# Performance work log

Hardware: AMD Instinct MI355X
Metric: run time of the kernel (lower is better)

The kernel has to match this reference:

```python
import jax, jax.numpy as jnp
import numpy as np

B, T, D_IN, D_SAE, K = 256, 8, 768, 8192, 32


def setup_inputs() -> dict:
    key = jax.random.key(0)
    k1, k2, k3 = jax.random.split(key, 3)
    x = jax.random.normal(k1, (B, T, D_IN), dtype=jnp.float32)
    # kaiming_uniform: bound = sqrt(6 / fan_in), fan_in = prod of trailing dims
    bound_e = float(np.sqrt(6.0 / (D_SAE * D_IN)))
    W_enc = jax.random.uniform(k2, (T, D_SAE, D_IN), jnp.float32, -bound_e, bound_e)
    bound_d = float(np.sqrt(6.0 / (D_IN * D_SAE)))
    W_dec = jax.random.uniform(k3, (T, D_IN, D_SAE), jnp.float32, -bound_d, bound_d)
    # decoder column normalization (norm over d_in axis), as in _normalize_decoder
    norms = jnp.clip(jnp.linalg.norm(W_dec, axis=1, keepdims=True), 1e-8)
    W_dec = W_dec / norms
    b_enc = jnp.zeros((T, D_SAE), jnp.float32)
    b_dec = jnp.zeros((T, D_IN), jnp.float32)
    return {"x": x, "W_enc": W_enc, "b_enc": b_enc, "W_dec": W_dec,
            "b_dec": b_dec, "k": K}


def reference(x, W_enc, b_enc, W_dec, b_dec, k):
    # x: (B, T, d_in)
    x_c = x - b_dec[None]                                   # (B, T, d)
    pre = jnp.einsum('btd,thd->bth', x_c, W_enc) + b_enc[None]  # (B, T, h)
    bt = pre.shape[0] * pre.shape[1]
    pre_flat = pre.reshape(bt, -1)
    topk_vals, topk_idx = jax.lax.top_k(pre_flat, k)        # (BT, k)
    rows = jnp.arange(bt)[:, None]
    u_flat = jnp.zeros_like(pre_flat).at[rows, topk_idx].set(jax.nn.relu(topk_vals))
    u = u_flat.reshape(pre.shape)                            # (B, T, h)
    x_hat = jnp.einsum('bth,tdh->btd', u, W_dec) + b_dec[None]
    recon_loss = jnp.mean(jnp.sum((x_hat - x) ** 2, axis=-1))
    return recon_loss, x_hat, u
```

## Files before the change

kernel.cpp:

```cpp
#include <hip/hip_runtime.h>
#include <cstdint>
#include <cstddef>

constexpr int B_SZ  = 256;
constexpr int T_SZ  = 8;
constexpr int DIN   = 768;
constexpr int DSAE  = 8192;
constexpr int KSEL  = 32;
constexpr int NROWS = B_SZ * T_SZ;
constexpr int CAND_CAP = 64;
constexpr int RCAP  = 32;
constexpr float EPS_W = 3.2e-4f;
constexpr int NSK   = DIN / 32;

constexpr size_t XC_SZ    = (size_t)NROWS * DIN;
constexpr size_t OFF_XC   = 0;
constexpr size_t OFF_XCP  = OFF_XC + XC_SZ;
constexpr size_t XCP_W    = XC_SZ / 2;
constexpr size_t OFF_SIDX = OFF_XCP + XCP_W;
constexpr size_t OFF_SVAL = OFF_SIDX + (size_t)NROWS * KSEL;
constexpr size_t OFF_BIG  = OFF_SVAL + (size_t)NROWS * KSEL;
constexpr size_t BIG_W    = (size_t)T_SZ * DSAE * DIN / 2;
constexpr size_t WS_FAST_WORDS = OFF_BIG + BIG_W;

typedef short bf16x8 __attribute__((ext_vector_type(8)));
typedef float f32x4  __attribute__((ext_vector_type(4)));

__device__ inline unsigned rne1(float x) {
  unsigned u = __float_as_uint(x);
  return (u + 0x7FFFu + ((u >> 16) & 1u)) >> 16;
}
__device__ inline float bf16tof(unsigned short v) {
  return __uint_as_float((unsigned)v << 16);
}
__device__ inline unsigned packtr(float a, float b) {
  return (__float_as_uint(a) >> 16) | (__float_as_uint(b) & 0xFFFF0000u);
}
__device__ inline void gload_lds16(const void* g, void* l) {
  __builtin_amdgcn_global_load_lds(
      (const __attribute__((address_space(1))) void*)g,
      (__attribute__((address_space(3))) void*)l, 16, 0, 0);
}

__global__ void k_zero(float* p) { *p = 0.f; }

__global__ __launch_bounds__(256) void k_xc(const float* __restrict__ x,
                                            const float* __restrict__ bdec,
                                            float* __restrict__ xc,
                                            unsigned short* __restrict__ xcp) {
  const int c = blockIdx.x * 256 + threadIdx.x;
  const int lane = c & 63;
  const int u = c >> 6;
  const int s  = u % NSK;
  const int tt = (u / NSK) & (T_SZ - 1);
  const int gm = u / (NSK * T_SZ);
  const int b  = gm * 16 + (lane & 15);
  const int k0 = s * 32 + (lane >> 4) * 8;
  const size_t rowOff = ((size_t)(b * T_SZ + tt)) * DIN + k0;
  float4 v0 = *(const float4*)(x + rowOff);
  float4 v1 = *(const float4*)(x + rowOff + 4);
  float4 d0 = *(const float4*)(bdec + tt * DIN + k0);
  float4 d1 = *(const float4*)(bdec + tt * DIN + k0 + 4);
  v0.x -= d0.x; v0.y -= d0.y; v0.z -= d0.z; v0.w -= d0.w;
  v1.x -= d1.x; v1.y -= d1.y; v1.z -= d1.z; v1.w -= d1.w;
  *(float4*)(xc + rowOff) = v0;
  *(float4*)(xc + rowOff + 4) = v1;
  uint4 p;
  p.x = rne1(v0.x) | (rne1(v0.y) << 16);
  p.y = rne1(v0.z) | (rne1(v0.w) << 16);
  p.z = rne1(v1.x) | (rne1(v1.y) << 16);
  p.w = rne1(v1.z) | (rne1(v1.w) << 16);
  *(uint4*)(xcp + (size_t)c * 8) = p;
}

__global__ __launch_bounds__(256, 2) void k_encoder(const unsigned short* __restrict__ xcp,
                                                    const float* __restrict__ Wenc,
                                                    const float* __restrict__ benc,
                                                    float* __restrict__ pre) {
  __shared__ __align__(16) float Bs[4][64 * 32];
  const int tid = threadIdx.x;
  const int wm = tid >> 6, lane = tid & 63;
  const int l15 = lane & 15, kc = lane >> 4;

  int gRow[2], gCol[2], ldsL[2];
#pragma unroll
  for (int i = 0; i < 2; ++i) {
    int L = i * 4096 + tid * 16;
    int G = L ^ (((L >> 7) & 7) << 4);
    gRow[i] = G >> 7;
    gCol[i] = (G & 127) >> 2;
    ldsL[i] = L;
  }
  int bOff0[4], bOff1[4];
#pragma unroll
  for (int ni = 0; ni < 4; ++ni) {
    int row = ni * 16 + l15;
    int P = row * 128 + kc * 32;
    int sw = (row & 7) << 4;
    bOff0[ni] = P ^ sw;
    bOff1[ni] = (P + 16) ^ sw;
  }
  constexpr size_t A_MI = (size_t)T_SZ * NSK * 512;

  for (int tile = 0; tile < 2; ++tile) {
    const int tileId = blockIdx.x + tile * 512;
    const int t  = tileId >> 7;
    const int n0 = (tileId & 127) * 64;

    const float* bG = Wenc + ((size_t)t * DSAE + n0) * DIN;
    const unsigned short* aP =
        xcp + ((size_t)(wm * 4 * T_SZ + t) * NSK) * 512 + lane * 8;

    auto STAGE = [&](int buf, int s) {
#pragma unroll
      for (int i = 0; i < 2; ++i)
        gload_lds16(bG + (size_t)gRow[i] * DIN + s * 32 + gCol[i],
                    (char*)&Bs[0][0] + buf * 8192 + ldsL[i]);
    };

    f32x4 acc[4][4] = {};
    bf16x8 aA[4], aB[4];
    STAGE(0, 0);
#pragma unroll
    for (int mi = 0; mi < 4; ++mi)
      aA[mi] = *(const bf16x8*)(aP + mi * A_MI);
    STAGE(1, 1);

#define ENC_W6 asm volatile("s_waitcnt vmcnt(6)" ::: "memory")
#define ENC_W4 asm volatile("s_waitcnt vmcnt(4)" ::: "memory")
#define ENC_W0 asm volatile("s_waitcnt vmcnt(0)" ::: "memory")
#define ENC_STEP(u, PFB, PFA, WAITOP) do {                                   \
    if (PFB) STAGE(((u) + 2) & 3, s0 + (u) + 2);                             \
    if (PFA) {                                                               \
      const unsigned short* ap = aP + (size_t)(s0 + (u) + 1) * 512;          \
      _Pragma("unroll")                                                      \
      for (int mi = 0; mi < 4; ++mi) {                                       \
        bf16x8 v = *(const bf16x8*)(ap + mi * A_MI);                         \
        if ((u) % 2 == 0) aB[mi] = v; else aA[mi] = v;                       \
      }                                                                      \
    }                                                                        \
    __builtin_amdgcn_sched_barrier(0);                                       \
    WAITOP;                                                                  \
    __builtin_amdgcn_s_barrier();                                            \
    __builtin_amdgcn_sched_barrier(0);                                       \
    {                                                                        \
      const char* bb = (const char*)&Bs[0][0] + ((u) & 3) * 8192;            \
      _Pragma("unroll")                                                      \
      for (int ni = 0; ni < 4; ++ni) {                                       \
        f32x4 f0 = *(const f32x4*)(bb + bOff0[ni]);                          \
        f32x4 f1 = *(const f32x4*)(bb + bOff1[ni]);                          \
        union { uint32_t w[4]; bf16x8 h; } cvu;                              \
        cvu.w[0] = packtr(f0.x, f0.y); cvu.w[1] = packtr(f0.z, f0.w);        \
        cvu.w[2] = packtr(f1.x, f1.y); cvu.w[3] = packtr(f1.z, f1.w);        \
        _Pragma("unroll")                                                    \
        for (int mi = 0; mi < 4; ++mi)                                       \
          acc[mi][ni] = __builtin_amdgcn_mfma_f32_16x16x32_bf16(             \
              ((u) % 2 == 0) ? aA[mi] : aB[mi], cvu.h, acc[mi][ni], 0, 0, 0);\
      }                                                                      \
    }                                                                        \
  } while (0)

    int s0 = 0;
    for (int g = 0; g < 5; ++g, s0 += 4) {
      ENC_STEP(0, true, true, ENC_W6); ENC_STEP(1, true, true, ENC_W6);
      ENC_STEP(2, true, true, ENC_W6); ENC_STEP(3, true, true, ENC_W6);
    }
    ENC_STEP(0, true, true, ENC_W6);  ENC_STEP(1, true, true, ENC_W6);
    ENC_STEP(2, false, true, ENC_W4); ENC_STEP(3, false, false, ENC_W0);
#undef ENC_STEP
#undef ENC_W6
#undef ENC_W4
#undef ENC_W0

#pragma unroll
    for (int ni = 0; ni < 4; ++ni) {
      const int col = n0 + ni * 16 + l15;
      const float bias = benc[(size_t)t * DSAE + col];
#pragma unroll
      for (int mi = 0; mi < 4; ++mi) {
        const int rbase = wm * 64 + mi * 16 + kc * 4;
#pragma unroll
        for (int j = 0; j < 4; ++j)
          pre[((size_t)(rbase + j) * T_SZ + t) * DSAE + col] = acc[mi][ni][j] + bias;
      }
    }
    if (tile == 0) __syncthreads();
  }
}

__global__ __launch_bounds__(256) void k_select(const float* __restrict__ xc,
                                                const float* __restrict__ Wenc,
                                                const float* __restrict__ benc,
                                                float* u,
                                                int* __restrict__ sel_idx,
                                                float* __restrict__ sel_val) {
  const int r = blockIdx.x, t = r & (T_SZ - 1);
  __shared__ float sp[DSAE];
  __shared__ float redf[4], redf2[4];
  __shared__ int   redi[4];
  __shared__ float cv[CAND_CAP]; __shared__ int ci[CAND_CAP];
  __shared__ float sv[CAND_CAP]; __shared__ int si[CAND_CAP];
  __shared__ float rv[RCAP];     __shared__ int ri[RCAP];
  __shared__ double rd[RCAP];
  __shared__ double xd[DIN];
  __shared__ int   s_n, s_nR, s_A, s_nW;
  const int tid = threadIdx.x, lane = tid & 63, w = tid >> 6;
  float* urow = u + (size_t)r * DSAE;

  float s1 = 0.f, s2 = 0.f;
  for (int sgm = 0; sgm < DSAE / 256; ++sgm) {
    float v = urow[tid + sgm * 256];
    sp[tid + sgm * 256] = v;
    s1 += v; s2 = fmaf(v, v, s2);
  }
  for (int off = 32; off; off >>= 1) {
    s1 += __shfl_down(s1, off); s2 += __shfl_down(s2, off);
  }
  if (lane == 0) { redf[w] = s1; redf2[w] = s2; }
  __syncthreads();
  const float mean = (redf[0] + redf[1] + redf[2] + redf[3]) * (1.f / DSAE);
  const float var  = (redf2[0] + redf2[1] + redf2[2] + redf2[3]) * (1.f / DSAE) - mean * mean;
  const float sd   = sqrtf(fmaxf(var, 1e-20f));

  auto countGE = [&](float th) -> int {
    int c = 0;
#pragma unroll
    for (int sgm = 0; sgm < DSAE / 256; ++sgm)
      c += (sp[tid + sgm * 256] >= th) ? 1 : 0;
    for (int off = 32; off; off >>= 1) c += __shfl_down(c, off);
    __syncthreads();
    if (lane == 0) redi[w] = c;
    __syncthreads();
    return redi[0] + redi[1] + redi[2] + redi[3];
  };

  float tlo = mean + 2.0f * sd, thi = mean + 3.5f * sd;
  for (int it = 0; it < 8 && countGE(tlo) < KSEL; ++it) tlo -= sd;
  float th = mean + 2.52f * sd;
  int c = countGE(th);
  for (int it = 0; it < 24 && (c < KSEL || c > CAND_CAP); ++it) {
    if (c > CAND_CAP) tlo = th; else thi = th;
    th = 0.5f * (tlo + thi);
    c = countGE(th);
  }
  if (c < KSEL) { th = tlo; c = countGE(th); }

  if (tid == 0) s_n = 0;
  __syncthreads();
  for (int sgm = 0; sgm < DSAE / 256; ++sgm) {
    int i = tid + sgm * 256;
    float v = sp[i];
    if (v >= th) {
      int p = atomicAdd(&s_n, 1);
      if (p < CAND_CAP) { cv[p] = v; ci[p] = i; }
    }
  }
  __syncthreads();
  const int n = s_n < CAND_CAP ? s_n : CAND_CAP;

  if (tid < n) {
    float v = cv[tid]; int id = ci[tid];
    int rk = 0;
    for (int j = 0; j < n; ++j) {
      float vj = cv[j];
      rk += (vj > v || (vj == v && ci[j] < id)) ? 1 : 0;
    }
    sv[rk] = v; si[rk] = id;
  }
  __syncthreads();

  const float v32 = sv[KSEL - 1];
  const float wlo = v32 - EPS_W, whi = v32 + EPS_W;
  if (tid == 0) {
    int A = 0;
    while (A < KSEL - 1 && sv[A] > whi) ++A;
    s_A = A;
    int e = A;
    while (e < n && sv[e] >= wlo) ++e;
    s_nW = e - A;
  }
  __syncthreads();
  const int A  = s_A;
  const int nW = s_nW < RCAP ? s_nW : RCAP;
  if (tid < nW) { rv[tid] = sv[A + tid]; ri[tid] = si[A + tid]; }
  if (tid == 0) s_nR = nW;
  __syncthreads();
  if (th > wlo) {
    for (int sgm = 0; sgm < DSAE / 256; ++sgm) {
      int i = tid + sgm * 256;
      float v = sp[i];
      if (v >= wlo && v < th) {
        int p = atomicAdd(&s_nR, 1);
        if (p < RCAP) { rv[p] = v; ri[p] = i; }
      }
    }
  }
  __syncthreads();
  const int nR = s_nR < RCAP ? s_nR : RCAP;

  if (nR >= 2) {
    for (int i = tid; i < DIN; i += 256) xd[i] = (double)xc[(size_t)r * DIN + i];
    __syncthreads();
    for (int j = w; j < nR; j += 4) {
      const int h = ri[j];
      const float* wrow = Wenc + ((size_t)t * DSAE + h) * DIN;
      double s = 0.0;
#pragma unroll
      for (int ss = 0; ss < DIN / 64; ++ss)
        s += xd[lane + 64 * ss] * (double)wrow[lane + 64 * ss];
      for (int off = 32; off; off >>= 1) s += __shfl_down(s, off);
      if (lane == 0) rd[j] = s + (double)benc[(size_t)t * DSAE + h];
    }
  } else if (nR == 1) {
    if (tid == 0) rd[0] = (double)rv[0];
  }
  __syncthreads();

  for (int sgm = 0; sgm < DSAE / 256; ++sgm) urow[tid + sgm * 256] = 0.f;
  __syncthreads();

  if (tid < A) {
    float val = fmaxf(sv[tid], 0.f);
    urow[si[tid]] = val;
    sel_idx[(size_t)r * KSEL + tid] = si[tid];
    sel_val[(size_t)r * KSEL + tid] = val;
  }
  const int need = KSEL - A;
  if (tid < nR) {
    double v = rd[tid]; int id = ri[tid];
    int rk = 0;
    for (int j = 0; j < nR; ++j) {
      double vj = rd[j];
      rk += (vj > v || (vj == v && ri[j] < id)) ? 1 : 0;
    }
    if (rk < need) {
      float val = fmaxf((float)v, 0.f);
      urow[id] = val;
      sel_idx[(size_t)r * KSEL + A + rk] = id;
      sel_val[(size_t)r * KSEL + A + rk] = val;
    }
  }
}

__global__ __launch_bounds__(256) void k_transpose(const float* __restrict__ W,
                                                   unsigned short* __restrict__ Wt) {
  __shared__ unsigned short tile[128 * 137];
  const int h0 = blockIdx.x * 128;
  const int d0 = blockIdx.y * 128;
  const int t  = blockIdx.z;
  const int tid = threadIdx.x;
  const float* src = W + ((size_t)t * DIN + d0) * DSAE + h0;

#pragma unroll
  for (int i = 0; i < 16; ++i) {
    const int F = (i * 256 + tid) * 4;
    const int r = F >> 7, c = F & 127;
    float4 v = *(const float4*)(src + (size_t)r * DSAE + c);
    unsigned short* p = &tile[r * 137 + c];
    p[0] = (unsigned short)rne1(v.x); p[1] = (unsigned short)rne1(v.y);
    p[2] = (unsigned short)rne1(v.z); p[3] = (unsigned short)rne1(v.w);
  }
  __syncthreads();

#pragma unroll
  for (int j = 0; j < 16; ++j) {
    const int E  = j * 256 + tid;
    const int hr = E >> 5;
    const int dc = (E & 31) * 4;
    unsigned a = (unsigned)tile[(dc + 0) * 137 + hr] |
                 ((unsigned)tile[(dc + 1) * 137 + hr] << 16);
    unsigned b = (unsigned)tile[(dc + 2) * 137 + hr] |
                 ((unsigned)tile[(dc + 3) * 137 + hr] << 16);
    uint2 o; o.x = a; o.y = b;
    *(uint2*)(Wt + ((size_t)(t * DSAE + h0 + hr)) * DIN + d0 + dc) = o;
  }
}

template <bool TRANSPOSED>
__global__ __launch_bounds__(256) void k_decoder(const void* __restrict__ Wd_,
                                                 const float* __restrict__ x,
                                                 const float* __restrict__ bdec,
                                                 const int* __restrict__ sel_idx,
                                                 const float* __restrict__ sel_val,
                                                 float* __restrict__ xhat,
                                                 float* __restrict__ loss) {
  const int r = blockIdx.x, t = r & (T_SZ - 1);
  __shared__ int   si[KSEL];
  __shared__ float sv[KSEL];
  __shared__ float rbuf[4];
  const int tid = threadIdx.x;
  if (tid < KSEL) {
    si[tid] = sel_idx[(size_t)r * KSEL + tid] & (DSAE - 1);
    sv[tid] = sel_val[(size_t)r * KSEL + tid];
  }
  __syncthreads();

  float acc[3];
#pragma unroll
  for (int i = 0; i < 3; ++i) acc[i] = bdec[(size_t)t * DIN + tid + 256 * i];
#pragma unroll 4
  for (int j = 0; j < KSEL; ++j) {
    const int h = si[j];
    const float v = sv[j];
    if (TRANSPOSED) {
      const unsigned short* wrow =
          (const unsigned short*)Wd_ + ((size_t)t * DSAE + h) * DIN;
#pragma unroll
      for (int i = 0; i < 3; ++i)
        acc[i] = fmaf(v, bf16tof(wrow[tid + 256 * i]), acc[i]);
    } else {
      const float* Wd = (const float*)Wd_;
#pragma unroll
      for (int i = 0; i < 3; ++i)
        acc[i] = fmaf(v, Wd[((size_t)t * DIN + tid + 256 * i) * DSAE + h], acc[i]);
    }
  }
  float sq = 0.f;
#pragma unroll
  for (int i = 0; i < 3; ++i) {
    const int d = tid + 256 * i;
    const float xv = x[(size_t)r * DIN + d];
    xhat[(size_t)r * DIN + d] = acc[i];
    const float e = acc[i] - xv;
    sq = fmaf(e, e, sq);
  }
  for (int off = 32; off; off >>= 1) sq += __shfl_down(sq, off);
  if ((tid & 63) == 0) rbuf[tid >> 6] = sq;
  __syncthreads();
  if (tid == 0)
    atomicAdd(loss, (rbuf[0] + rbuf[1] + rbuf[2] + rbuf[3]) * (1.0f / NROWS));
}

extern "C" void kernel_launch(void* const* d_in, const int* in_sizes, int n_in,
                              void* d_out, int out_size, void* d_ws, size_t ws_size,
                              hipStream_t stream) {
  const float* x    = (const float*)d_in[0];
  const float* Wenc = (const float*)d_in[1];
  const float* benc = (const float*)d_in[2];
  const float* Wdec = (const float*)d_in[3];
  const float* bdec = (const float*)d_in[4];

  float* out  = (float*)d_out;
  float* loss = out;
  float* xhat = out + 1;
  float* u    = out + 1 + (size_t)NROWS * DIN;

  float*          wsf  = (float*)d_ws;
  float*          xc   = wsf + OFF_XC;
  unsigned short* xcp  = (unsigned short*)(wsf + OFF_XCP);
  int*            sidx = (int*)(wsf + OFF_SIDX);
  float*          sval = wsf + OFF_SVAL;
  unsigned short* big  = (unsigned short*)(wsf + OFF_BIG);
  const bool fast = ws_size >= WS_FAST_WORDS * sizeof(float);

  k_zero<<<1, 1, 0, stream>>>(loss);
  k_xc<<<NROWS * DIN / (256 * 8), 256, 0, stream>>>(x, bdec, xc, xcp);
  k_encoder<<<512, 256, 0, stream>>>(xcp, Wenc, benc, u);
  k_select<<<NROWS, 256, 0, stream>>>(xc, Wenc, benc, u, sidx, sval);
  if (fast) {
    k_transpose<<<dim3(DSAE / 128, DIN / 128, T_SZ), 256, 0, stream>>>(Wdec, big);
    k_decoder<true><<<NROWS, 256, 0, stream>>>(big, x, bdec, sidx, sval, xhat, loss);
  } else {
    k_decoder<false><<<NROWS, 256, 0, stream>>>(Wdec, x, bdec, sidx, sval, xhat, loss);
  }
}
```

Baseline: 239.4 us.

## Store encoder pre-activations as bf16 scratch and zero u in separate kernel

The encoder now writes pre-activations as bf16 into a workspace buffer instead of fp32 into the output u, which halves the write and the re-read traffic in the select kernel. Select reads the packed bf16 rows with vector loads, and u is cleared by a standalone vectorized zero kernel instead of a per-row zero pass after selection. The candidate margin EPS_W is widened to absorb bf16 rounding, so more candidates may need the exact fp64 rescoring path. The workspace grows by an NROWS×DSAE bf16 buffer.

Measured after the change: 234.0 us. 2.3% less time.

```diff
diff --git a/kernel.cpp b/kernel.cpp
--- a/kernel.cpp
+++ b/kernel.cpp
@@ -10,7 +10,7 @@
 constexpr int NROWS = B_SZ * T_SZ;
 constexpr int CAND_CAP = 64;
 constexpr int RCAP  = 32;
-constexpr float EPS_W = 3.2e-4f;
+constexpr float EPS_W = 5.5e-4f;
 constexpr int NSK   = DIN / 32;
 
 constexpr size_t XC_SZ    = (size_t)NROWS * DIN;
@@ -19,7 +19,9 @@
 constexpr size_t XCP_W    = XC_SZ / 2;
 constexpr size_t OFF_SIDX = OFF_XCP + XCP_W;
 constexpr size_t OFF_SVAL = OFF_SIDX + (size_t)NROWS * KSEL;
-constexpr size_t OFF_BIG  = OFF_SVAL + (size_t)NROWS * KSEL;
+constexpr size_t OFF_PREB = OFF_SVAL + (size_t)NROWS * KSEL;
+constexpr size_t PREB_W   = (size_t)NROWS * DSAE / 2;
+constexpr size_t OFF_BIG  = OFF_PREB + PREB_W;
 constexpr size_t BIG_W    = (size_t)T_SZ * DSAE * DIN / 2;
 constexpr size_t WS_FAST_WORDS = OFF_BIG + BIG_W;
 
@@ -43,6 +45,14 @@
 }
 
 __global__ void k_zero(float* p) { *p = 0.f; }
+
+__global__ __launch_bounds__(256) void k_uzero(float* __restrict__ u) {
+  const size_t base = (size_t)(blockIdx.x * 256 + threadIdx.x) * 4;
+  const size_t stride = (size_t)gridDim.x * 256 * 4;
+  const float4 z = {0.f, 0.f, 0.f, 0.f};
+  for (size_t i = base; i < (size_t)NROWS * DSAE; i += stride)
+    *(float4*)(u + i) = z;
+}
 
 __global__ __launch_bounds__(256) void k_xc(const float* __restrict__ x,
                                             const float* __restrict__ bdec,
@@ -76,7 +86,7 @@
 __global__ __launch_bounds__(256, 2) void k_encoder(const unsigned short* __restrict__ xcp,
                                                     const float* __restrict__ Wenc,
                                                     const float* __restrict__ benc,
-                                                    float* __restrict__ pre) {
+                                                    unsigned short* __restrict__ preb) {
   __shared__ __align__(16) float Bs[4][64 * 32];
   const int tid = threadIdx.x;
   const int wm = tid >> 6, lane = tid & 63;
@@ -181,7 +191,8 @@
         const int rbase = wm * 64 + mi * 16 + kc * 4;
 #pragma unroll
         for (int j = 0; j < 4; ++j)
-          pre[((size_t)(rbase + j) * T_SZ + t) * DSAE + col] = acc[mi][ni][j] + bias;
+          preb[((size_t)(rbase + j) * T_SZ + t) * DSAE + col] =
+              (unsigned short)rne1(acc[mi][ni][j] + bias);
       }
     }
     if (tile == 0) __syncthreads();
@@ -191,7 +202,8 @@
 __global__ __launch_bounds__(256) void k_select(const float* __restrict__ xc,
                                                 const float* __restrict__ Wenc,
                                                 const float* __restrict__ benc,
-                                                float* u,
+                                                const unsigned short* __restrict__ preb,
+                                                float* __restrict__ u,
                                                 int* __restrict__ sel_idx,
                                                 float* __restrict__ sel_val) {
   const int r = blockIdx.x, t = r & (T_SZ - 1);
@@ -205,13 +217,21 @@
   __shared__ double xd[DIN];
   __shared__ int   s_n, s_nR, s_A, s_nW;
   const int tid = threadIdx.x, lane = tid & 63, w = tid >> 6;
-  float* urow = u + (size_t)r * DSAE;
 
   float s1 = 0.f, s2 = 0.f;
-  for (int sgm = 0; sgm < DSAE / 256; ++sgm) {
-    float v = urow[tid + sgm * 256];
-    sp[tid + sgm * 256] = v;
-    s1 += v; s2 = fmaf(v, v, s2);
+#pragma unroll
+  for (int sgm = 0; sgm < 4; ++sgm) {
+    const int i0 = sgm * 2048 + tid * 8;
+    uint4 pk = *(const uint4*)(preb + (size_t)r * DSAE + i0);
+    const unsigned wds[4] = {pk.x, pk.y, pk.z, pk.w};
+#pragma unroll
+    for (int q = 0; q < 4; ++q) {
+      float lo = __uint_as_float(wds[q] << 16);
+      float hi = __uint_as_float(wds[q] & 0xFFFF0000u);
+      sp[i0 + q * 2 + 0] = lo;
+      sp[i0 + q * 2 + 1] = hi;
+      s1 += lo + hi; s2 = fmaf(lo, lo, fmaf(hi, hi, s2));
+    }
   }
   for (int off = 32; off; off >>= 1) {
     s1 += __shfl_down(s1, off); s2 += __shfl_down(s2, off);
@@ -316,9 +336,7 @@
   }
   __syncthreads();
 
-  for (int sgm = 0; sgm < DSAE / 256; ++sgm) urow[tid + sgm * 256] = 0.f;
-  __syncthreads();
-
+  float* urow = u + (size_t)r * DSAE;
   if (tid < A) {
     float val = fmaxf(sv[tid], 0.f);
     urow[si[tid]] = val;
@@ -350,7 +368,6 @@
   const int t  = blockIdx.z;
   const int tid = threadIdx.x;
   const float* src = W + ((size_t)t * DIN + d0) * DSAE + h0;
-
 #pragma unroll
   for (int i = 0; i < 16; ++i) {
     const int F = (i * 256 + tid) * 4;
@@ -361,7 +378,6 @@
     p[2] = (unsigned short)rne1(v.z); p[3] = (unsigned short)rne1(v.w);
   }
   __syncthreads();
-
 #pragma unroll
   for (int j = 0; j < 16; ++j) {
     const int E  = j * 256 + tid;
@@ -450,13 +466,15 @@
   unsigned short* xcp  = (unsigned short*)(wsf + OFF_XCP);
   int*            sidx = (int*)(wsf + OFF_SIDX);
   float*          sval = wsf + OFF_SVAL;
+  unsigned short* preb = (unsigned short*)(wsf + OFF_PREB);
   unsigned short* big  = (unsigned short*)(wsf + OFF_BIG);
   const bool fast = ws_size >= WS_FAST_WORDS * sizeof(float);
 
   k_zero<<<1, 1, 0, stream>>>(loss);
+  k_uzero<<<2048, 256, 0, stream>>>(u);
   k_xc<<<NROWS * DIN / (256 * 8), 256, 0, stream>>>(x, bdec, xc, xcp);
-  k_encoder<<<512, 256, 0, stream>>>(xcp, Wenc, benc, u);
-  k_select<<<NROWS, 256, 0, stream>>>(xc, Wenc, benc, u, sidx, sval);
+  k_encoder<<<512, 256, 0, stream>>>(xcp, Wenc, benc, preb);
+  k_select<<<NROWS, 256, 0, stream>>>(xc, Wenc, benc, preb, u, sidx, sval);
   if (fast) {
     k_transpose<<<dim3(DSAE / 128, DIN / 128, T_SZ), 256, 0, stream>>>(Wdec, big);
     k_decoder<true><<<NROWS, 256, 0, stream>>>(big, x, bdec, sidx, sval, xhat, loss);
```
